# Kernel optimization log

Measured on AMD Instinct MI355X. Metric: run time of the kernel, lower is better.

## Reference

```python
import jax, jax.numpy as jnp
import numpy as np

RENDER_SIZE = 256   # renderer image_size
IMG_H, IMG_W = 480, 640
ORIG_SIZE = 640     # max(H, W)
SIGMA = 0.5         # soft-silhouette sharpness in pixels (approximates NR hard rasterizer)
CHUNK = 128         # faces per scan step (bounds peak memory)
N_VERTS = 2048
N_FACES = 4096


def _se3_exp(dof):
    """dof = [v(3), omega(3)] (pytorch3d order) -> (R [3,3], t [3]) column convention."""
    v, w = dof[:3], dof[3:]
    th2 = jnp.sum(w * w)
    th = jnp.sqrt(th2 + 1e-30)
    small = th < 1e-4
    th_s = jnp.where(small, 1.0, th)          # safe denom (avoids nan grads)
    th2_s = jnp.where(small, 1.0, th2)
    A = jnp.where(small, 1.0 - th2 / 6.0, jnp.sin(th_s) / th_s)
    B = jnp.where(small, 0.5 - th2 / 24.0, (1.0 - jnp.cos(th_s)) / th2_s)
    C = jnp.where(small, 1.0 / 6.0 - th2 / 120.0, (th_s - jnp.sin(th_s)) / (th2_s * th_s))
    Kx = jnp.array([[0.0, -w[2], w[1]], [w[2], 0.0, -w[0]], [-w[1], w[0], 0.0]], dtype=dof.dtype)
    K2 = Kx @ Kx
    I = jnp.eye(3, dtype=dof.dtype)
    R = I + A * Kx + B * K2
    V = I + B * Kx + C * K2   # left Jacobian
    return R, V @ v


def _cross2(u, w):
    return u[..., 0] * w[..., 1] - u[..., 1] * w[..., 0]


def _rasterize_silhouette(tri):
    """tri: [F,3,2] projected triangle verts in render-pixel coords -> [R,R] coverage."""
    P = RENDER_SIZE * RENDER_SIZE
    ys, xs = jnp.meshgrid(jnp.arange(RENDER_SIZE, dtype=jnp.float32) + 0.5,
                          jnp.arange(RENDER_SIZE, dtype=jnp.float32) + 0.5, indexing='ij')
    px, py = xs.reshape(-1), ys.reshape(-1)  # [P] pixel centers
    tris = tri.reshape(N_FACES // CHUNK, CHUNK, 3, 2)

    def body(logp, t3):
        a = t3                          # [C,3,2] edge start verts
        e = jnp.roll(t3, -1, axis=1) - a  # [C,3,2] edge vectors (v1-v0, v2-v1, v0-v2)
        area2 = _cross2(e[:, 0], -e[:, 2])            # signed doubled area, [C]
        sgn = jnp.where(area2 >= 0, 1.0, -1.0)        # winding fix so inside > 0
        elen = jnp.sqrt(jnp.sum(e * e, -1)) + 1e-9    # [C,3]
        c0 = e[..., 0] * a[..., 1] - e[..., 1] * a[..., 0]  # [C,3]
        # signed distance of each pixel to each edge line: [P,C,3]
        d = (e[None, :, :, 0] * py[:, None, None] - e[None, :, :, 1] * px[:, None, None] - c0[None]) / elen[None]
        d = sgn[None, :, None] * d
        dmin = jnp.min(d, axis=2)                     # [P,C] min edge distance
        s = jnp.minimum(jax.nn.sigmoid(dmin / SIGMA), 1.0 - 1e-6)
        return logp + jnp.sum(jnp.log1p(-s), axis=1), None

    logp, _ = jax.lax.scan(body, jnp.zeros(P, jnp.float32), tris)
    return (1.0 - jnp.exp(logp)).reshape(RENDER_SIZE, RENDER_SIZE)


def _resize_nearest(img, size):
    return jax.image.resize(img, (size, size), method='nearest')


def reference(dof, vertices, faces, K, mask_gt):
    R, t = _se3_exp(dof)
    cam = vertices @ R.T + t              # [N,3] camera coords
    uvw = cam @ K.T                       # pinhole projection
    xy = uvw[:, :2] / uvw[:, 2:3]         # pixel coords at orig_size resolution
    xy = xy * (RENDER_SIZE / ORIG_SIZE)   # scale to render grid
    tri = xy[faces]                       # [F,3,2]
    si = _rasterize_silhouette(tri)       # [R,R]
    si = _resize_nearest(si, ORIG_SIZE)[:IMG_H, :IMG_W]
    loss = jnp.sum((si - mask_gt) ** 2)
    return loss, si


def setup_inputs() -> dict:
    key = jax.random.key(0)
    k1, k2, k3, k4 = jax.random.split(key, 4)
    v = jax.random.normal(k1, (N_VERTS, 3), dtype=jnp.float32)
    vertices = 0.5 * v / (jnp.linalg.norm(v, axis=1, keepdims=True) + 1e-8)  # unit-ish sphere mesh
    faces = jax.random.randint(k2, (N_FACES, 3), 0, N_VERTS, dtype=jnp.int32)
    # pose: object ~2.5m in front of camera, small rotation + noise
    dof = jnp.array([0.0, 0.0, 2.5, 0.2, -0.1, 0.15], dtype=jnp.float32) \
          + 0.05 * jax.random.normal(k3, (6,), dtype=jnp.float32)
    K = jnp.array([[600.0, 0.0, 320.0], [0.0, 600.0, 240.0], [0.0, 0.0, 1.0]], dtype=jnp.float32)
    mask_gt = (jax.random.uniform(k4, (IMG_H, IMG_W)) < 0.3).astype(jnp.float32)
    return {"dof": dof, "vertices": vertices, "faces": faces, "K": K, "mask_gt": mask_gt}
```

## Files before the change

kernel.cpp:

```cpp
#include <hip/hip_runtime.h>
#include <math.h>

#define RENDER 256
#define IMG_H 480
#define IMG_W 640
#define NV 2048
#define NF 4096
#define FACE_SLICES 16
#define FACES_PER_SLICE (NF / FACE_SLICES)
#define TILES 256
#define N_UNITS (TILES * FACE_SLICES)

#define SIGMA_INV 2.0f
#define CAP 13.815510557964274f
#define LOG2E 1.4426950408889634f
#define ZK 2.8853900817779268f
#define CAP2 19.931568569324174f
#define ECAP 999999.0f
#define SKIP_PIX -26.0f

#define WS_FD_OFF    0
#define WS_LOGP_OFF  (192 * 1024)

__global__ __launch_bounds__(256) void k_prep(const float* __restrict__ dof,
                                              const float* __restrict__ verts,
                                              const int* __restrict__ faces,
                                              const float* __restrict__ Km,
                                              float* __restrict__ fdata,
                                              float* __restrict__ logp,
                                              float* __restrict__ out) {
    if (blockIdx.x >= 16) {
        logp[(blockIdx.x - 16) * 256 + threadIdx.x] = 0.0f;
        if (blockIdx.x == 16 && threadIdx.x == 0) out[0] = 0.0f;
        return;
    }

    __shared__ float sxy[NV * 2];

    float v0 = dof[0], v1 = dof[1], v2 = dof[2];
    float w0 = dof[3], w1 = dof[4], w2 = dof[5];
    float th2 = w0 * w0 + w1 * w1 + w2 * w2;
    float th = sqrtf(th2 + 1e-30f);
    bool small = th < 1e-4f;
    float th_s = small ? 1.0f : th;
    float th2_s = small ? 1.0f : th2;
    float A = small ? (1.0f - th2 / 6.0f) : (sinf(th_s) / th_s);
    float B = small ? (0.5f - th2 / 24.0f) : ((1.0f - cosf(th_s)) / th2_s);
    float C = small ? (1.0f / 6.0f - th2 / 120.0f)
                    : ((th_s - sinf(th_s)) / (th2_s * th_s));
    float Kx[9] = {0.0f, -w2, w1, w2, 0.0f, -w0, -w1, w0, 0.0f};
    float w[3] = {w0, w1, w2};
    float R[9], V[9];
    for (int i = 0; i < 3; i++)
        for (int j = 0; j < 3; j++) {
            float K2 = w[i] * w[j] - (i == j ? th2 : 0.0f);
            float id = (i == j) ? 1.0f : 0.0f;
            R[i * 3 + j] = id + A * Kx[i * 3 + j] + B * K2;
            V[i * 3 + j] = id + B * Kx[i * 3 + j] + C * K2;
        }
    float t0 = V[0] * v0 + V[1] * v1 + V[2] * v2;
    float t1 = V[3] * v0 + V[4] * v1 + V[5] * v2;
    float t2 = V[6] * v0 + V[7] * v1 + V[8] * v2;
    float K00 = Km[0], K01 = Km[1], K02 = Km[2];
    float K10 = Km[3], K11 = Km[4], K12 = Km[5];
    float K20 = Km[6], K21 = Km[7], K22 = Km[8];
    const float scale = 256.0f / 640.0f;

    for (int n = threadIdx.x; n < NV; n += 256) {
        float vx = verts[n * 3], vy = verts[n * 3 + 1], vz = verts[n * 3 + 2];
        float cx = R[0] * vx + R[1] * vy + R[2] * vz + t0;
        float cy = R[3] * vx + R[4] * vy + R[5] * vz + t1;
        float cz = R[6] * vx + R[7] * vy + R[8] * vz + t2;
        float u = K00 * cx + K01 * cy + K02 * cz;
        float v = K10 * cx + K11 * cy + K12 * cz;
        float ww = K20 * cx + K21 * cy + K22 * cz;
        float rw = __builtin_amdgcn_rcpf(ww) * scale;
        sxy[n * 2]     = u * rw;
        sxy[n * 2 + 1] = v * rw;
    }
    __syncthreads();

    int f = blockIdx.x * 256 + threadIdx.x;
    int i0 = faces[f * 3], i1 = faces[f * 3 + 1], i2 = faces[f * 3 + 2];
    float x0 = sxy[i0 * 2], y0 = sxy[i0 * 2 + 1];
    float x1 = sxy[i1 * 2], y1 = sxy[i1 * 2 + 1];
    float x2 = sxy[i2 * 2], y2 = sxy[i2 * 2 + 1];
    float ex[3] = {x1 - x0, x2 - x1, x0 - x2};
    float ey[3] = {y1 - y0, y2 - y1, y0 - y2};
    float ax[3] = {x0, x1, x2};
    float ay[3] = {y0, y1, y2};
    float area2 = ex[0] * (-ey[2]) - ey[0] * (-ex[2]);
    float sgn = (area2 >= 0.0f) ? 1.0f : -1.0f;
    float* o = fdata + f * 12;
    for (int k = 0; k < 3; k++) {
        float elen = sqrtf(ex[k] * ex[k] + ey[k] * ey[k]) + 1e-9f;
        float c0 = ex[k] * ay[k] - ey[k] * ax[k];
        float inv = sgn / elen * ZK;
        float Ac = ex[k] * inv;
        float Bc = -ey[k] * inv;
        o[k * 4 + 0] = Ac;
        o[k * 4 + 1] = Bc;
        o[k * 4 + 2] = -c0 * inv;
        o[k * 4 + 3] = 7.5f * (fabsf(Ac) + fabsf(Bc));
    }
}

__global__ __launch_bounds__(256) void k_raster(const float* __restrict__ fdata,
                                                float* __restrict__ logp) {
    __shared__ float s_data[4096];
    __shared__ int s_n;
    __shared__ int s_ncap;
    const int tid = threadIdx.x;
    if (tid == 0) { s_n = 0; s_ncap = 0; }
    __syncthreads();

    const int unit = (blockIdx.x * 2053) & (N_UNITS - 1);
    const int tile = unit >> 4;
    const int slice = unit & 15;
    const int tileX = tile & 15;
    const int tileY = tile >> 4;
    const float cx = tileX * 16 + 8.0f;
    const float cy = tileY * 16 + 8.0f;
    const float4* __restrict__ fd4 = (const float4*)fdata;

    {
        int f = slice * FACES_PER_SLICE + tid;
        float4 e0 = fd4[f * 3 + 0];
        float4 e1 = fd4[f * 3 + 1];
        float4 e2 = fd4[f * 3 + 2];
        float d0 = fmaf(e0.y, cx, fmaf(e0.x, cy, e0.z));
        float d1 = fmaf(e1.y, cx, fmaf(e1.x, cy, e1.z));
        float d2 = fmaf(e2.y, cx, fmaf(e2.x, cy, e2.z));
        float capm = fminf(d0 - e0.w, fminf(d1 - e1.w, d2 - e2.w));
        float skpm = fminf(d0 + e0.w, fminf(d1 + e1.w, d2 + e2.w));
        bool capped = capm > CAP2;
        bool live = (!capped) && (skpm > SKIP_PIX);
        unsigned long long mcap = __ballot(capped);
        unsigned long long mliv = __ballot(live);
        int lane = tid & 63;
        int base = 0;
        if (lane == 0) {
            base = atomicAdd(&s_n, __popcll(mliv));
            atomicAdd(&s_ncap, __popcll(mcap));
        }
        base = __shfl(base, 0, 64);
        if (live) {
            int pos = base + __popcll(mliv & ((1ull << lane) - 1ull));
            float4* dst = (float4*)(s_data + pos * 12);
            dst[0] = e0; dst[1] = e1; dst[2] = e2;
        }
    }
    __syncthreads();

    const int n = s_n;
    const int ncap = s_ncap;
    if (n == 0 && ncap == 0) return;

    const int wv = tid >> 6;
    const int lane = tid & 63;
    const int row = lane >> 2;
    const int col0 = lane & 3;
    const float py = (float)(tileY * 16 + row) + 0.5f;
    const float px0 = (float)(tileX * 16 + col0) + 0.5f;

    float pm[4] = {1.0f, 1.0f, 1.0f, 1.0f};
    int   pe[4] = {0, 0, 0, 0};
    const float4* sd = (const float4*)s_data;
    if (wv < n) {
        float4 c0 = sd[wv * 3 + 0], c1 = sd[wv * 3 + 1], c2 = sd[wv * 3 + 2];
        int it = 0;
        for (int i = wv; i < n; i += 4) {
            float4 n0 = sd[(i + 4) * 3 + 0];
            float4 n1 = sd[(i + 4) * 3 + 1];
            float4 n2 = sd[(i + 4) * 3 + 2];
            float t0p = fmaf(c0.x, py, c0.z);
            float t1p = fmaf(c1.x, py, c1.z);
            float t2p = fmaf(c2.x, py, c2.z);
            #pragma unroll
            for (int k = 0; k < 4; ++k) {
                float px = px0 + (float)(4 * k);
                float z = fminf(fmaf(c0.y, px, t0p),
                          fminf(fmaf(c1.y, px, t1p), fmaf(c2.y, px, t2p)));
                float e = fminf(__builtin_amdgcn_exp2f(z), ECAP);
                pm[k] = fmaf(pm[k], e, pm[k]);
            }
            if (((++it) & 3) == 0) {
                #pragma unroll
                for (int k = 0; k < 4; ++k) {
                    unsigned b = __float_as_uint(pm[k]);
                    pe[k] += (int)(b >> 23) - 127;
                    pm[k] = __uint_as_float((b & 0x007fffffu) | 0x3f800000u);
                }
            }
            c0 = n0; c1 = n1; c2 = n2;
        }
    }
    float acc[4];
    #pragma unroll
    for (int k = 0; k < 4; ++k)
        acc[k] = -((float)pe[k] + __builtin_amdgcn_logf(pm[k]));

    __syncthreads();
    {
        int base = wv * 1024 + row * 16 + col0;
        s_data[base + 0]  = acc[0];
        s_data[base + 4]  = acc[1];
        s_data[base + 8]  = acc[2];
        s_data[base + 12] = acc[3];
    }
    __syncthreads();
    {
        int p = tid;
        float v = s_data[p] + s_data[1024 + p] + s_data[2048 + p] +
                  s_data[3072 + p] - CAP2 * (float)ncap;
        int iyp = tileY * 16 + (p >> 4);
        int ixp = tileX * 16 + (p & 15);
        atomicAdd(&logp[iyp * RENDER + ixp], v);
    }
}

__global__ __launch_bounds__(256) void k_final(const float* __restrict__ logp,
                                               const float* __restrict__ mask,
                                               float* __restrict__ out) {
    int idx = blockIdx.x * 256 + threadIdx.x;
    int r = idx / IMG_W;
    int c = idx - r * IMG_W;
    int ir = (2 * r + 1) / 5;
    int ic = (2 * c + 1) / 5;
    float si = 1.0f - __builtin_amdgcn_exp2f(logp[ir * RENDER + ic]);
    out[1 + idx] = si;
    float diff = si - mask[idx];
    float d2 = diff * diff;
    #pragma unroll
    for (int off = 32; off > 0; off >>= 1) d2 += __shfl_down(d2, off, 64);
    __shared__ float sred[4];
    int lane = threadIdx.x & 63;
    int wv = threadIdx.x >> 6;
    if (lane == 0) sred[wv] = d2;
    __syncthreads();
    if (threadIdx.x == 0)
        atomicAdd(out, sred[0] + sred[1] + sred[2] + sred[3]);
}

extern "C" void kernel_launch(void* const* d_in, const int* in_sizes, int n_in,
                              void* d_out, int out_size, void* d_ws, size_t ws_size,
                              hipStream_t stream) {
    const float* dof   = (const float*)d_in[0];
    const float* verts = (const float*)d_in[1];
    const int*   faces = (const int*)d_in[2];
    const float* Km    = (const float*)d_in[3];
    const float* mask  = (const float*)d_in[4];
    float* out = (float*)d_out;

    char* ws = (char*)d_ws;
    float* fdata = (float*)(ws + WS_FD_OFF);
    float* logp  = (float*)(ws + WS_LOGP_OFF);

    k_prep<<<272, 256, 0, stream>>>(dof, verts, faces, Km, fdata, logp, out);
    k_raster<<<N_UNITS, 256, 0, stream>>>(fdata, logp);
    k_final<<<(IMG_H * IMG_W) / 256, 256, 0, stream>>>(logp, mask, out);
}
```

Measured before the change: 104.0 us.

## Add dilated per-face bounding boxes to cull faces and halve face slices

The prep kernel now computes, for each face, a bounding box of the triangle dilated outward along its edge normals, and writes it to a new workspace buffer. The raster kernel tests each face's box against the tile before loading its 48-byte edge data, so faces outside the tile cost only one float4 load. Face slices drop from 16 to 8, so each block handles 512 faces in two passes with a larger shared buffer. This halves the block count and per-block setup, but adds shared-memory pressure, more serial work per block, and a possible overflow if many faces stay live.

```diff
diff --git a/kernel.cpp b/kernel.cpp
--- a/kernel.cpp
+++ b/kernel.cpp
@@ -6,7 +6,7 @@
 #define IMG_W 640
 #define NV 2048
 #define NF 4096
-#define FACE_SLICES 16
+#define FACE_SLICES 8
 #define FACES_PER_SLICE (NF / FACE_SLICES)
 #define TILES 256
 #define N_UNITS (TILES * FACE_SLICES)
@@ -18,15 +18,18 @@
 #define CAP2 19.931568569324174f
 #define ECAP 999999.0f
 #define SKIP_PIX -26.0f
+#define DILATE 9.1f
 
 #define WS_FD_OFF    0
-#define WS_LOGP_OFF  (192 * 1024)
+#define WS_BB_OFF    (192 * 1024)
+#define WS_LOGP_OFF  (256 * 1024)
 
 __global__ __launch_bounds__(256) void k_prep(const float* __restrict__ dof,
                                               const float* __restrict__ verts,
                                               const int* __restrict__ faces,
                                               const float* __restrict__ Km,
                                               float* __restrict__ fdata,
+                                              float* __restrict__ bbox,
                                               float* __restrict__ logp,
                                               float* __restrict__ out) {
     if (blockIdx.x >= 16) {
@@ -87,61 +90,94 @@
     float x2 = sxy[i2 * 2], y2 = sxy[i2 * 2 + 1];
     float ex[3] = {x1 - x0, x2 - x1, x0 - x2};
     float ey[3] = {y1 - y0, y2 - y1, y0 - y2};
-    float ax[3] = {x0, x1, x2};
-    float ay[3] = {y0, y1, y2};
+    float axv[3] = {x0, x1, x2};
+    float ayv[3] = {y0, y1, y2};
     float area2 = ex[0] * (-ey[2]) - ey[0] * (-ex[2]);
     float sgn = (area2 >= 0.0f) ? 1.0f : -1.0f;
     float* o = fdata + f * 12;
+    float nux[3], nuy[3];
     for (int k = 0; k < 3; k++) {
         float elen = sqrtf(ex[k] * ex[k] + ey[k] * ey[k]) + 1e-9f;
-        float c0 = ex[k] * ay[k] - ey[k] * ax[k];
-        float inv = sgn / elen * ZK;
+        float c0 = ex[k] * ayv[k] - ey[k] * axv[k];
+        float inv_e = sgn / elen;
+        float inv = inv_e * ZK;
         float Ac = ex[k] * inv;
         float Bc = -ey[k] * inv;
         o[k * 4 + 0] = Ac;
         o[k * 4 + 1] = Bc;
         o[k * 4 + 2] = -c0 * inv;
         o[k * 4 + 3] = 7.5f * (fabsf(Ac) + fabsf(Bc));
-    }
+        nux[k] = -ey[k] * inv_e;
+        nuy[k] =  ex[k] * inv_e;
+    }
+    float bx0 = 1e30f, by0 = 1e30f, bx1 = -1e30f, by1 = -1e30f;
+    float msum = 0.0f;
+    for (int k = 0; k < 3; k++) {
+        int km = k ? (k - 1) : 2;
+        float det = nux[km] * nuy[k] - nuy[km] * nux[k];
+        float invd = 1.0f / det;
+        float mx = (nuy[km] - nuy[k]) * invd;
+        float my = (nux[k] - nux[km]) * invd;
+        msum += fabsf(mx) + fabsf(my);
+        float vxo = axv[k] + DILATE * mx;
+        float vyo = ayv[k] + DILATE * my;
+        bx0 = fminf(bx0, vxo); bx1 = fmaxf(bx1, vxo);
+        by0 = fminf(by0, vyo); by1 = fmaxf(by1, vyo);
+    }
+    if (!(msum < 1e7f)) {
+        bx0 = -1e9f; by0 = -1e9f; bx1 = 1e9f; by1 = 1e9f;
+    }
+    ((float4*)bbox)[f] = make_float4(bx0, by0, bx1, by1);
 }
 
 __global__ __launch_bounds__(256) void k_raster(const float* __restrict__ fdata,
+                                                const float* __restrict__ bbox,
                                                 float* __restrict__ logp) {
-    __shared__ float s_data[4096];
+    __shared__ float s_data[6208];
     __shared__ int s_n;
     __shared__ int s_ncap;
     const int tid = threadIdx.x;
     if (tid == 0) { s_n = 0; s_ncap = 0; }
     __syncthreads();
 
-    const int unit = (blockIdx.x * 2053) & (N_UNITS - 1);
-    const int tile = unit >> 4;
-    const int slice = unit & 15;
+    const int unit = (blockIdx.x * 1141) & (N_UNITS - 1);
+    const int tile = unit >> 3;
+    const int slice = unit & 7;
     const int tileX = tile & 15;
     const int tileY = tile >> 4;
     const float cx = tileX * 16 + 8.0f;
     const float cy = tileY * 16 + 8.0f;
+    const float tx0c = tileX * 16 + 0.5f, tx1c = tileX * 16 + 15.5f;
+    const float ty0c = tileY * 16 + 0.5f, ty1c = tileY * 16 + 15.5f;
     const float4* __restrict__ fd4 = (const float4*)fdata;
-
-    {
-        int f = slice * FACES_PER_SLICE + tid;
-        float4 e0 = fd4[f * 3 + 0];
-        float4 e1 = fd4[f * 3 + 1];
-        float4 e2 = fd4[f * 3 + 2];
-        float d0 = fmaf(e0.y, cx, fmaf(e0.x, cy, e0.z));
-        float d1 = fmaf(e1.y, cx, fmaf(e1.x, cy, e1.z));
-        float d2 = fmaf(e2.y, cx, fmaf(e2.x, cy, e2.z));
-        float capm = fminf(d0 - e0.w, fminf(d1 - e1.w, d2 - e2.w));
-        float skpm = fminf(d0 + e0.w, fminf(d1 + e1.w, d2 + e2.w));
-        bool capped = capm > CAP2;
-        bool live = (!capped) && (skpm > SKIP_PIX);
+    const float4* __restrict__ bb4 = (const float4*)bbox;
+    const int lane = tid & 63;
+
+    for (int j = 0; j < 2; ++j) {
+        int f = slice * FACES_PER_SLICE + j * 256 + tid;
+        float4 bb = bb4[f];
+        bool inbb = (bb.z >= tx0c) & (bb.x <= tx1c) &
+                    (bb.w >= ty0c) & (bb.y <= ty1c);
+        bool capped = false, live = false;
+        float4 e0, e1, e2;
+        if (inbb) {
+            e0 = fd4[f * 3 + 0];
+            e1 = fd4[f * 3 + 1];
+            e2 = fd4[f * 3 + 2];
+            float d0 = fmaf(e0.y, cx, fmaf(e0.x, cy, e0.z));
+            float d1 = fmaf(e1.y, cx, fmaf(e1.x, cy, e1.z));
+            float d2 = fmaf(e2.y, cx, fmaf(e2.x, cy, e2.z));
+            float capm = fminf(d0 - e0.w, fminf(d1 - e1.w, d2 - e2.w));
+            float skpm = fminf(d0 + e0.w, fminf(d1 + e1.w, d2 + e2.w));
+            capped = capm > CAP2;
+            live = (!capped) && (skpm > SKIP_PIX);
+        }
         unsigned long long mcap = __ballot(capped);
         unsigned long long mliv = __ballot(live);
-        int lane = tid & 63;
         int base = 0;
         if (lane == 0) {
             base = atomicAdd(&s_n, __popcll(mliv));
-            atomicAdd(&s_ncap, __popcll(mcap));
+            if (mcap) atomicAdd(&s_ncap, __popcll(mcap));
         }
         base = __shfl(base, 0, 64);
         if (live) {
@@ -157,7 +193,6 @@
     if (n == 0 && ncap == 0) return;
 
     const int wv = tid >> 6;
-    const int lane = tid & 63;
     const int row = lane >> 2;
     const int col0 = lane & 3;
     const float py = (float)(tileY * 16 + row) + 0.5f;
@@ -254,9 +289,10 @@
 
     char* ws = (char*)d_ws;
     float* fdata = (float*)(ws + WS_FD_OFF);
+    float* bbox  = (float*)(ws + WS_BB_OFF);
     float* logp  = (float*)(ws + WS_LOGP_OFF);
 
-    k_prep<<<272, 256, 0, stream>>>(dof, verts, faces, Km, fdata, logp, out);
-    k_raster<<<N_UNITS, 256, 0, stream>>>(fdata, logp);
+    k_prep<<<272, 256, 0, stream>>>(dof, verts, faces, Km, fdata, bbox, logp, out);
+    k_raster<<<N_UNITS, 256, 0, stream>>>(fdata, bbox, logp);
     k_final<<<(IMG_H * IMG_W) / 256, 256, 0, stream>>>(logp, mask, out);
 }
```

Result: slower. 114.0 us (+9.6%).
